# Optimization experiments

Measured on AMD Instinct MI355X. Metric: run time of the kernel, lower is better.

## Reference

```python
import jax, jax.numpy as jnp
import numpy as np

D_MODEL = 2048
NUM_HEADS = 16
D_K = D_MODEL // NUM_HEADS
THETA = 10000.0
BATCH, SEQ = 2, 2048


def setup_inputs() -> dict:
    key = jax.random.key(0)
    ks = jax.random.split(key, 5)
    scale = 1.0 / np.sqrt(D_MODEL)
    x = jax.random.normal(ks[0], (BATCH, SEQ, D_MODEL), dtype=jnp.float32)
    token_positions = jnp.broadcast_to(jnp.arange(SEQ, dtype=jnp.int32)[None, :], (BATCH, SEQ))
    Wq = jax.random.normal(ks[1], (D_MODEL, D_MODEL), dtype=jnp.float32) * scale
    Wk = jax.random.normal(ks[2], (D_MODEL, D_MODEL), dtype=jnp.float32) * scale
    Wv = jax.random.normal(ks[3], (D_MODEL, D_MODEL), dtype=jnp.float32) * scale
    Wo = jax.random.normal(ks[4], (D_MODEL, D_MODEL), dtype=jnp.float32) * scale
    return {"x": x, "token_positions": token_positions, "Wq": Wq, "Wk": Wk, "Wv": Wv, "Wo": Wo}


def _apply_rope(t, positions):
    # t: [b, h, s, d_k]; positions: [b, s]. Interleaved-pair rotation.
    half = D_K // 2
    inv_freq = THETA ** (-jnp.arange(0, half, dtype=jnp.float32) * 2.0 / D_K)  # [half]
    ang = positions.astype(jnp.float32)[:, :, None] * inv_freq[None, None, :]  # [b, s, half]
    cos = jnp.cos(ang)[:, None, :, :]  # [b, 1, s, half]
    sin = jnp.sin(ang)[:, None, :, :]
    t2 = t.reshape(*t.shape[:-1], half, 2)
    x1, x2 = t2[..., 0], t2[..., 1]
    r1 = x1 * cos - x2 * sin
    r2 = x1 * sin + x2 * cos
    return jnp.stack([r1, r2], axis=-1).reshape(t.shape)


def reference(x, token_positions, Wq, Wk, Wv, Wo):
    b, s, _ = x.shape
    # Linear layers compute x @ W^T (weight stored as [out, in], no bias)
    def proj(w):
        y = jnp.einsum('bsd,ed->bse', x, w)
        return y.reshape(b, s, NUM_HEADS, D_K).transpose(0, 2, 1, 3)  # b h s d
    Q, K, V = proj(Wq), proj(Wk), proj(Wv)
    Q = _apply_rope(Q, token_positions)
    K = _apply_rope(K, token_positions)
    scores = jnp.einsum('bhqd,bhkd->bhqk', Q, K) / jnp.sqrt(jnp.float32(D_K))
    causal = jnp.tril(jnp.ones((s, s), dtype=bool))
    scores = jnp.where(causal[None, None], scores, jnp.finfo(scores.dtype).min)
    attn = jax.nn.softmax(scores, axis=-1)
    out = jnp.einsum('bhqk,bhkd->bhqd', attn, V)  # b h s d
    out = out.transpose(0, 2, 1, 3).reshape(b, s, D_MODEL)
    return jnp.einsum('bse,de->bsd', out, Wo)
```

## Files before the change

### kernel.cpp

```cpp
#include <hip/hip_runtime.h>
#include <cstdint>
#include <cstddef>

#define D_MODEL 2048
#define NHEAD 16
#define DK 128
#define SEQ 2048
#define BATCH 2
#define NTOK (BATCH * SEQ)
#define NQB 32

typedef __bf16 bf16;
typedef __bf16 bf16x2 __attribute__((ext_vector_type(2)));
typedef __bf16 bf16x4 __attribute__((ext_vector_type(4)));
typedef __bf16 bf16x8 __attribute__((ext_vector_type(8)));
typedef float f32x4 __attribute__((ext_vector_type(4)));

__device__ __forceinline__ void g2lds16(const void* g, void* l) {
  __builtin_amdgcn_global_load_lds(
      (const __attribute__((address_space(1))) void*)g,
      (__attribute__((address_space(3))) void*)l, 16, 0, 0);
}

__device__ __forceinline__ void cstore(float* p, float v) { *p = v; }
__device__ __forceinline__ void cstore(bf16* p, float v) { *p = (bf16)v; }

#define BAR()                              \
  {                                        \
    asm volatile("" ::: "memory");         \
    __builtin_amdgcn_s_barrier();          \
    asm volatile("" ::: "memory");         \
  }

__global__ void k_conv5(const float* __restrict__ X, const float* __restrict__ W0,
                        const float* __restrict__ W1, const float* __restrict__ W2,
                        const float* __restrict__ W3, bf16* __restrict__ xo,
                        bf16* __restrict__ o0, bf16* __restrict__ o1,
                        bf16* __restrict__ o2, bf16* __restrict__ o3,
                        int nx4, int nw4) {
  const float* in;
  bf16* out;
  int n;
  switch (blockIdx.y) {
    case 0: in = X; out = xo; n = nx4; break;
    case 1: in = W0; out = o0; n = nw4; break;
    case 2: in = W1; out = o1; n = nw4; break;
    case 3: in = W2; out = o2; n = nw4; break;
    default: in = W3; out = o3; n = nw4;
  }
  int i = blockIdx.x * blockDim.x + threadIdx.x;
  if (i >= n) return;
  const float4 v = ((const float4*)in)[i];
  bf16x4 o = {(bf16)v.x, (bf16)v.y, (bf16)v.z, (bf16)v.w};
  ((bf16x4*)out)[i] = o;
}

__global__ __launch_bounds__(512, 1) void k_gemm8(
    const bf16* __restrict__ A, const bf16* __restrict__ B0p, const bf16* __restrict__ B1p,
    const bf16* __restrict__ B2p, bf16* __restrict__ C0, bf16* __restrict__ C1,
    bf16* __restrict__ C2, const int* __restrict__ pos, int M, int N, int K) {
  const bf16* Bp = B0p;
  bf16* Cp = C0;
  if (blockIdx.z == 1) { Bp = B1p; Cp = C1; }
  else if (blockIdx.z == 2) { Bp = B2p; Cp = C2; }
  const bool rope = (blockIdx.z < 2);

  __shared__ bf16 Ab[2][256 * 64];
  __shared__ bf16 Bb[2][256 * 64];

  const int t = threadIdx.x;
  const int wid = t >> 6, lane = t & 63;
  const int wr = wid >> 2, wc = wid & 3;
  const int lr = lane & 15, lg = lane >> 4;
  const int bm = blockIdx.y, bn = blockIdx.x;
  const size_t arow0 = (size_t)bm * 256;
  const size_t brow0 = (size_t)bn * 256;

  const int srow = wid * 8 + (lane >> 3);
  const int schunk = ((lane & 7) ^ ((lane >> 3) & 7)) * 8;

#define STG(X, row0, k0, lb, h)                                                \
  {                                                                            \
    g2lds16(&(X)[((row0) + (h)*128 + srow) * (size_t)K + (k0) + schunk],       \
            &(lb)[((h)*128 + wid * 8) * 64]);                                  \
    g2lds16(&(X)[((row0) + (h)*128 + 64 + srow) * (size_t)K + (k0) + schunk],  \
            &(lb)[((h)*128 + 64 + wid * 8) * 64]);                             \
  }
#define LDA8(lb, mh, m, kk) \
  (*(const bf16x8*)&(lb)[((mh)*128 + wr * 64 + (m)*16 + lr) * 64 + ((((kk)*4 + lg) ^ (lr & 7)) * 8)])
#define LDB8(lb, nh, n, kk) \
  (*(const bf16x8*)&(lb)[((nh)*128 + wc * 32 + (n)*16 + lr) * 64 + ((((kk)*4 + lg) ^ (lr & 7)) * 8)])

  const int T = K >> 6;

  STG(A, arow0, 0, Ab[0], 0);
  STG(A, arow0, 0, Ab[0], 1);
  STG(Bp, brow0, 0, Bb[0], 0);
  STG(Bp, brow0, 0, Bb[0], 1);
  STG(A, arow0, 64, Ab[1], 0);

  f32x4 acc[2][2][4][2] = {};

  for (int tt = 0; tt < T; ++tt) {
    const int cur = tt & 1;
    const bf16* Ac = Ab[cur];
    const bf16* Bc = Bb[cur];
    bf16* Aw = Ab[cur];
    bf16* An = Ab[cur ^ 1];
    bf16* Bn = Bb[cur ^ 1];
    const int k1 = (tt + 1) << 6;
    const int k2 = (tt + 2) << 6;
    const bool pf1 = (tt + 1 < T);
    const bool pf2 = (tt + 2 < T);

    if (tt == T - 1) {
      asm volatile("s_waitcnt vmcnt(0)" ::: "memory");
    } else {
      asm volatile("s_waitcnt vmcnt(2)" ::: "memory");
    }
    BAR();

    bf16x8 a[4][2], b0[2][2], b1[2][2];

#pragma unroll
    for (int m = 0; m < 4; ++m)
#pragma unroll
      for (int kk = 0; kk < 2; ++kk) a[m][kk] = LDA8(Ac, 0, m, kk);
#pragma unroll
    for (int n = 0; n < 2; ++n)
#pragma unroll
      for (int kk = 0; kk < 2; ++kk) b0[n][kk] = LDB8(Bc, 0, n, kk);
    if (pf1) {
      STG(A, arow0, k1, An, 1);
      STG(Bp, brow0, k1, Bn, 0);
    }
    __builtin_amdgcn_s_setprio(1);
#pragma unroll
    for (int m = 0; m < 4; ++m)
#pragma unroll
      for (int n = 0; n < 2; ++n)
#pragma unroll
        for (int kk = 0; kk < 2; ++kk)
          acc[0][0][m][n] =
              __builtin_amdgcn_mfma_f32_16x16x32_bf16(a[m][kk], b0[n][kk], acc[0][0][m][n], 0, 0, 0);
    __builtin_amdgcn_s_setprio(0);
    BAR();

#pragma unroll
    for (int n = 0; n < 2; ++n)
#pragma unroll
      for (int kk = 0; kk < 2; ++kk) b1[n][kk] = LDB8(Bc, 1, n, kk);
    if (pf1) STG(Bp, brow0, k1, Bn, 1);
    __builtin_amdgcn_s_setprio(1);
#pragma unroll
    for (int m = 0; m < 4; ++m)
#pragma unroll
      for (int n = 0; n < 2; ++n)
#pragma unroll
        for (int kk = 0; kk < 2; ++kk)
          acc[0][1][m][n] =
              __builtin_amdgcn_mfma_f32_16x16x32_bf16(a[m][kk], b1[n][kk], acc[0][1][m][n], 0, 0, 0);
    __builtin_amdgcn_s_setprio(0);

#pragma unroll
    for (int m = 0; m < 4; ++m)
#pragma unroll
      for (int kk = 0; kk < 2; ++kk) a[m][kk] = LDA8(Ac, 1, m, kk);
    if (pf2) STG(A, arow0, k2, Aw, 0);
    __builtin_amdgcn_s_setprio(1);
#pragma unroll
    for (int m = 0; m < 4; ++m)
#pragma unroll
      for (int n = 0; n < 2; ++n)
#pragma unroll
        for (int kk = 0; kk < 2; ++kk)
          acc[1][1][m][n] =
              __builtin_amdgcn_mfma_f32_16x16x32_bf16(a[m][kk], b1[n][kk], acc[1][1][m][n], 0, 0, 0);

#pragma unroll
    for (int m = 0; m < 4; ++m)
#pragma unroll
      for (int n = 0; n < 2; ++n)
#pragma unroll
        for (int kk = 0; kk < 2; ++kk)
          acc[1][0][m][n] =
              __builtin_amdgcn_mfma_f32_16x16x32_bf16(a[m][kk], b0[n][kk], acc[1][0][m][n], 0, 0, 0);
    __builtin_amdgcn_s_setprio(0);
  }

  float invf[2];
#pragma unroll
  for (int n = 0; n < 2; ++n) {
    int f = ((wc * 32 + n * 16 + lr) & 127) >> 1;
    invf[n] = exp2f((float)f * -0.20762050593121503f);
  }
#pragma unroll
  for (int mh = 0; mh < 2; ++mh)
#pragma unroll
    for (int m = 0; m < 4; ++m) {
      size_t rowb = arow0 + mh * 128 + wr * 64 + m * 16 + lg * 4;
#pragma unroll
      for (int r = 0; r < 4; ++r) {
        float p = rope ? (float)pos[rowb + r] : 0.0f;
#pragma unroll
        for (int n = 0; n < 2; ++n) {
          float sn, cs;
          if (rope) __sincosf(p * invf[n], &sn, &cs);
#pragma unroll
          for (int nh = 0; nh < 2; ++nh) {
            float v = acc[mh][nh][m][n][r];
            float vp = __shfl_xor(v, 1);
            float outv = v;
            if (rope) outv = (lr & 1) ? (v * cs + vp * sn) : (v * cs - vp * sn);
            size_t col = brow0 + nh * 128 + wc * 32 + n * 16 + lr;
            Cp[(rowb + r) * N + col] = (bf16)outv;
          }
        }
      }
    }
#undef STG
#undef LDA8
#undef LDB8
}

__global__ __launch_bounds__(512, 1) void k_gemmPV(
    const bf16* __restrict__ A, const bf16* __restrict__ Bp, bf16* __restrict__ Cp,
    int M, int N, int K) {
  const int wg = blockIdx.x;
  const int bn = wg & 7;
  const int bm = wg >> 3;

  __shared__ bf16 Ab[2][128 * 64];
  __shared__ bf16 Bb[2][256 * 64];

  const int t = threadIdx.x;
  const int wid = t >> 6, lane = t & 63;
  const int wr = wid >> 2, wc = wid & 3;
  const int lr = lane & 15, lg = lane >> 4;
  const size_t arow0 = (size_t)bm * 128;
  const size_t brow0 = (size_t)bn * 256;

  const int srow = wid * 8 + (lane >> 3);
  const int schunk = ((lane & 7) ^ ((lane >> 3) & 7)) * 8;

#define STGA(X, k0, lb, h) \
  g2lds16(&(X)[(arow0 + (h)*64 + srow) * (size_t)K + (k0) + schunk], &(lb)[((h)*64 + wid * 8) * 64]);
#define STGB(X, k0, lb, h)                                                        \
  {                                                                               \
    g2lds16(&(X)[(brow0 + (h)*128 + srow) * (size_t)K + (k0) + schunk],           \
            &(lb)[((h)*128 + wid * 8) * 64]);                                     \
    g2lds16(&(X)[(brow0 + (h)*128 + 64 + srow) * (size_t)K + (k0) + schunk],      \
            &(lb)[((h)*128 + 64 + wid * 8) * 64]);                                \
  }
#define LDA8(lb, mh, m, kk) \
  (*(const bf16x8*)&(lb)[((mh)*64 + wr * 32 + (m)*16 + lr) * 64 + ((((kk)*4 + lg) ^ (lr & 7)) * 8)])
#define LDB8(lb, nh, n, kk) \
  (*(const bf16x8*)&(lb)[((nh)*128 + wc * 32 + (n)*16 + lr) * 64 + ((((kk)*4 + lg) ^ (lr & 7)) * 8)])

  const int T = K >> 6;

  STGA(A, 0, Ab[0], 0);
  STGA(A, 0, Ab[0], 1);
  STGB(Bp, 0, Bb[0], 0);
  STGB(Bp, 0, Bb[0], 1);
  STGA(A, 64, Ab[1], 0);

  f32x4 acc[2][2][2][2] = {};

  for (int tt = 0; tt < T; ++tt) {
    const int cur = tt & 1;
    const bf16* Ac = Ab[cur];
    const bf16* Bc = Bb[cur];
    bf16* Aw = Ab[cur];
    bf16* An = Ab[cur ^ 1];
    bf16* Bn = Bb[cur ^ 1];
    const int k1 = (tt + 1) << 6;
    const int k2 = (tt + 2) << 6;
    const bool pf1 = (tt + 1 < T);
    const bool pf2 = (tt + 2 < T);

    if (tt == T - 1) {
      asm volatile("s_waitcnt vmcnt(0)" ::: "memory");
    } else {
      asm volatile("s_waitcnt vmcnt(1)" ::: "memory");
    }
    BAR();

    bf16x8 a[2][2], b[2][2];

#pragma unroll
    for (int m = 0; m < 2; ++m)
#pragma unroll
      for (int kk = 0; kk < 2; ++kk) a[m][kk] = LDA8(Ac, 0, m, kk);
#pragma unroll
    for (int n = 0; n < 2; ++n)
#pragma unroll
      for (int kk = 0; kk < 2; ++kk) b[n][kk] = LDB8(Bc, 0, n, kk);
    if (pf1) {
      STGA(A, k1, An, 1);
      STGB(Bp, k1, Bn, 0);
    }
    __builtin_amdgcn_s_setprio(1);
#pragma unroll
    for (int m = 0; m < 2; ++m)
#pragma unroll
      for (int n = 0; n < 2; ++n)
#pragma unroll
        for (int kk = 0; kk < 2; ++kk)
          acc[0][0][m][n] =
              __builtin_amdgcn_mfma_f32_16x16x32_bf16(a[m][kk], b[n][kk], acc[0][0][m][n], 0, 0, 0);
    __builtin_amdgcn_s_setprio(0);
    BAR();

#pragma unroll
    for (int n = 0; n < 2; ++n)
#pragma unroll
      for (int kk = 0; kk < 2; ++kk) b[n][kk] = LDB8(Bc, 1, n, kk);
    if (pf1) STGB(Bp, k1, Bn, 1);
    __builtin_amdgcn_s_setprio(1);
#pragma unroll
    for (int m = 0; m < 2; ++m)
#pragma unroll
      for (int n = 0; n < 2; ++n)
#pragma unroll
        for (int kk = 0; kk < 2; ++kk)
          acc[0][1][m][n] =
              __builtin_amdgcn_mfma_f32_16x16x32_bf16(a[m][kk], b[n][kk], acc[0][1][m][n], 0, 0, 0);
    __builtin_amdgcn_s_setprio(0);
    BAR();

#pragma unroll
    for (int m = 0; m < 2; ++m)
#pragma unroll
      for (int kk = 0; kk < 2; ++kk) a[m][kk] = LDA8(Ac, 1, m, kk);
    if (pf2) STGA(A, k2, Aw, 0);
    __builtin_amdgcn_s_setprio(1);
#pragma unroll
    for (int m = 0; m < 2; ++m)
#pragma unroll
      for (int n = 0; n < 2; ++n)
#pragma unroll
        for (int kk = 0; kk < 2; ++kk)
          acc[1][1][m][n] =
              __builtin_amdgcn_mfma_f32_16x16x32_bf16(a[m][kk], b[n][kk], acc[1][1][m][n], 0, 0, 0);
    __builtin_amdgcn_s_setprio(0);
    BAR();

#pragma unroll
    for (int n = 0; n < 2; ++n)
#pragma unroll
      for (int kk = 0; kk < 2; ++kk) b[n][kk] = LDB8(Bc, 0, n, kk);
    __builtin_amdgcn_s_setprio(1);
#pragma unroll
    for (int m = 0; m < 2; ++m)
#pragma unroll
      for (int n = 0; n < 2; ++n)
#pragma unroll
        for (int kk = 0; kk < 2; ++kk)
          acc[1][0][m][n] =
              __builtin_amdgcn_mfma_f32_16x16x32_bf16(a[m][kk], b[n][kk], acc[1][0][m][n], 0, 0, 0);
    __builtin_amdgcn_s_setprio(0);
  }

#pragma unroll
  for (int mh = 0; mh < 2; ++mh)
#pragma unroll
    for (int nh = 0; nh < 2; ++nh)
#pragma unroll
      for (int m = 0; m < 2; ++m) {
        size_t rowb = arow0 + mh * 64 + wr * 32 + m * 16 + lg * 4;
#pragma unroll
        for (int n = 0; n < 2; ++n) {
          size_t col = brow0 + nh * 128 + wc * 32 + n * 16 + lr;
#pragma unroll
          for (int r = 0; r < 4; ++r) Cp[(rowb + r) * N + col] = (bf16)acc[mh][nh][m][n][r];
        }
      }
#undef STGA
#undef STGB
#undef LDA8
#undef LDB8
}

template <typename OutT>
__global__ __launch_bounds__(256, 2) void k_gemm_nt(
    const bf16* __restrict__ A, const bf16* __restrict__ B0, const bf16* __restrict__ B1,
    const bf16* __restrict__ B2, OutT* __restrict__ C0, OutT* __restrict__ C1,
    OutT* __restrict__ C2, int M, int N, int K) {
  const bf16* Bp = B0;
  OutT* Cp = C0;
  if (blockIdx.z == 1) { Bp = B1; Cp = C1; }
  else if (blockIdx.z == 2) { Bp = B2; Cp = C2; }

  __shared__ bf16 As[128 * 32];
  __shared__ bf16 Bs[128 * 32];

  const int t = threadIdx.x;
  const int w = t >> 6;
  const int lane = t & 63;
  const int lr = lane & 15;
  const int lg = lane >> 4;
  const int wr = w >> 1, wc = w & 1;
  const int bm = blockIdx.y, bn = blockIdx.x;

  f32x4 acc[4][4] = {};

  const int srow = lane >> 2;
  const int scol = (lane & 3) * 8;

  const int kt_iters = K >> 5;
  for (int kt = 0; kt < kt_iters; ++kt) {
    const int kbase = kt * 32;
#pragma unroll
    for (int i = 0; i < 2; ++i) {
      int chunk = w * 2 + i;
      int row = chunk * 16 + srow;
      g2lds16(&A[(size_t)(bm * 128 + row) * K + kbase + scol], &As[chunk * 512]);
      g2lds16(&Bp[(size_t)(bn * 128 + row) * K + kbase + scol], &Bs[chunk * 512]);
    }
    asm volatile("s_waitcnt vmcnt(0)" ::: "memory");
    __syncthreads();

    bf16x8 af[4], bfr[4];
#pragma unroll
    for (int m = 0; m < 4; ++m)
      af[m] = *(const bf16x8*)&As[(wr * 64 + m * 16 + lr) * 32 + lg * 8];
#pragma unroll
    for (int n = 0; n < 4; ++n)
      bfr[n] = *(const bf16x8*)&Bs[(wc * 64 + n * 16 + lr) * 32 + lg * 8];
#pragma unroll
    for (int m = 0; m < 4; ++m)
#pragma unroll
      for (int n = 0; n < 4; ++n)
        acc[m][n] = __builtin_amdgcn_mfma_f32_16x16x32_bf16(af[m], bfr[n], acc[m][n], 0, 0, 0);
    __syncthreads();
  }

#pragma unroll
  for (int m = 0; m < 4; ++m) {
    int rowb = bm * 128 + wr * 64 + m * 16 + lg * 4;
#pragma unroll
    for (int n = 0; n < 4; ++n) {
      int col = bn * 128 + wc * 64 + n * 16 + lr;
#pragma unroll
      for (int r = 0; r < 4; ++r) cstore(&Cp[(size_t)(rowb + r) * N + col], acc[m][n][r]);
    }
  }
}

__global__ __launch_bounds__(256, 2) void k_attn(const bf16* __restrict__ Q,
                                                 const bf16* __restrict__ K,
                                                 const bf16* __restrict__ V,
                                                 bf16* __restrict__ O) {
  const int wg = blockIdx.x;
  const int g = wg & 7;
  const int i = wg >> 3;
  const int bh = g + 8 * (i & 3);
  const int pr = i >> 2;
  const int b = bh >> 4, h = bh & 15;

  const int t = threadIdx.x;
  const int w = t >> 6, lane = t & 63;
  const int lr = lane & 15, lg = lane >> 4;

  const size_t rowbase = (size_t)b * SEQ;
  const int hoff = h * DK;

  __shared__ bf16 Ks[2][64 * 128];
  __shared__ uint32_t VTu[2][128 * 32];
  __shared__ bf16 Pb[4][16 * 64];

  const int kp = t & 31;
  const int d0s = (t >> 5) * 16;

  const float scale = 0.08838834764831845f;
  const float FIXM = 8.0f;

  bf16x8 sa0, sa1, sb0, sb1;
  int cur = 0;

  const int krow_l = lane >> 4;
  const int kchunk = lane & 15;

  for (int qsel = 0; qsel < 2; ++qsel) {
    const int qblk = qsel ? pr : (NQB - 1 - pr);
    const int qb = qblk * 64;
    const int ktiles = qblk + 1;

    bf16x8 qf[4];
    {
      size_t qrow = rowbase + qb + w * 16 + lr;
#pragma unroll
      for (int c = 0; c < 4; ++c)
        qf[c] = *(const bf16x8*)&Q[qrow * D_MODEL + hoff + c * 32 + lg * 8];
    }

    f32x4 o[8] = {};
    f32x4 lrow = {};

#pragma unroll
    for (int j = 0; j < 4; ++j) {
      int row = w * 16 + j * 4 + krow_l;
      int chunk = kchunk ^ (j * 4 + krow_l);
      g2lds16(&K[(rowbase + row) * D_MODEL + hoff + chunk * 8],
              &Ks[cur][(size_t)(w * 16 + j * 4) * 128]);
    }
    {
      const bf16* vp0 = &V[(rowbase + 2 * kp) * D_MODEL + hoff + d0s];
      sa0 = *(const bf16x8*)vp0;
      sa1 = *(const bf16x8*)(vp0 + 8);
      sb0 = *(const bf16x8*)(vp0 + D_MODEL);
      sb1 = *(const bf16x8*)(vp0 + D_MODEL + 8);
    }

    for (int kt = 0; kt < ktiles; ++kt) {
      const int k0 = kt * 64;
#pragma unroll
      for (int j = 0; j < 8; ++j) {
        int d = d0s + j;
        bf16x2 p0 = {sa0[j], sb0[j]};
        VTu[cur][d * 32 + (kp ^ ((d & 7) << 2))] = *(const uint32_t*)&p0;
      }
#pragma unroll
      for (int j = 0; j < 8; ++j) {
        int d = d0s + 8 + j;
        bf16x2 p1 = {sa1[j], sb1[j]};
        VTu[cur][d * 32 + (kp ^ ((d & 7) << 2))] = *(const uint32_t*)&p1;
      }
      asm volatile("s_waitcnt vmcnt(0)" ::: "memory");
      __syncthreads();

      if (kt + 1 < ktiles) {
#pragma unroll
        for (int j = 0; j < 4; ++j) {
          int row = w * 16 + j * 4 + krow_l;
          int chunk = kchunk ^ (j * 4 + krow_l);
          g2lds16(&K[(rowbase + k0 + 64 + row) * D_MODEL + hoff + chunk * 8],
                  &Ks[cur ^ 1][(size_t)(w * 16 + j * 4) * 128]);
        }
        const bf16* vp0 = &V[(rowbase + k0 + 64 + 2 * kp) * D_MODEL + hoff + d0s];
        sa0 = *(const bf16x8*)vp0;
        sa1 = *(const bf16x8*)(vp0 + 8);
        sb0 = *(const bf16x8*)(vp0 + D_MODEL);
        sb1 = *(const bf16x8*)(vp0 + D_MODEL + 8);
      }

      f32x4 sc[4];
      __builtin_amdgcn_s_setprio(1);
#pragma unroll
      for (int tt = 0; tt < 4; ++tt) {
        f32x4 a = {};
#pragma unroll
        for (int c = 0; c < 4; ++c) {
          bf16x8 kf = *(const bf16x8*)&Ks[cur][(tt * 16 + lr) * 128 + (((c * 4 + lg) ^ lr) * 8)];
          a = __builtin_amdgcn_mfma_f32_16x16x32_bf16(qf[c], kf, a, 0, 0, 0);
        }
        sc[tt] = a * scale;
      }
      __builtin_amdgcn_s_setprio(0);

      const int qrow0 = qb + w * 16 + lg * 4;
      if (k0 + 64 > qb + w * 16) {
#pragma unroll
        for (int tt = 0; tt < 4; ++tt) {
          int kcol = k0 + tt * 16 + lr;
#pragma unroll
          for (int r = 0; r < 4; ++r)
            if (kcol > qrow0 + r) sc[tt][r] = -3.0e38f;
        }
      }

#pragma unroll
      for (int tt = 0; tt < 4; ++tt)
#pragma unroll
        for (int r = 0; r < 4; ++r) {
          float p = __expf(sc[tt][r] - FIXM);
          sc[tt][r] = p;
          lrow[r] += p;
        }

#pragma unroll
      for (int tt = 0; tt < 4; ++tt)
#pragma unroll
        for (int r = 0; r < 4; ++r) {
          int q = lg * 4 + r;
          int col = tt * 16 + lr;
          Pb[w][q * 64 + (col ^ ((q & 7) << 3))] = (bf16)sc[tt][r];
        }
      asm volatile("s_waitcnt lgkmcnt(0)" ::: "memory");
      bf16x8 pf0 = *(const bf16x8*)&Pb[w][lr * 64 + ((lg * 8) ^ ((lr & 7) << 3))];
      bf16x8 pf1 = *(const bf16x8*)&Pb[w][lr * 64 + ((32 + lg * 8) ^ ((lr & 7) << 3))];

      __builtin_amdgcn_s_setprio(1);
#pragma unroll
      for (int nt = 0; nt < 8; ++nt) {
        int d = nt * 16 + lr;
        bf16x8 vf0 = *(const bf16x8*)&VTu[cur][d * 32 + ((lg * 4) ^ ((d & 7) << 2))];
        bf16x8 vf1 = *(const bf16x8*)&VTu[cur][d * 32 + ((16 + lg * 4) ^ ((d & 7) << 2))];
        o[nt] = __builtin_amdgcn_mfma_f32_16x16x32_bf16(pf0, vf0, o[nt], 0, 0, 0);
        o[nt] = __builtin_amdgcn_mfma_f32_16x16x32_bf16(pf1, vf1, o[nt], 0, 0, 0);
      }
      __builtin_amdgcn_s_setprio(0);
      cur ^= 1;
    }

#pragma unroll
    for (int off = 8; off >= 1; off >>= 1)
#pragma unroll
      for (int r = 0; r < 4; ++r) lrow[r] += __shfl_xor(lrow[r], off);

    size_t orow = rowbase + qb + w * 16 + lg * 4;
#pragma unroll
    for (int nt = 0; nt < 8; ++nt)
#pragma unroll
      for (int r = 0; r < 4; ++r)
        O[(orow + r) * D_MODEL + hoff + nt * 16 + lr] = (bf16)(o[nt][r] / lrow[r]);
  }
}

extern "C" void kernel_launch(void* const* d_in, const int* in_sizes, int n_in, void* d_out,
                              int out_size, void* d_ws, size_t ws_size, hipStream_t stream) {
  const float* x = (const float*)d_in[0];
  const int* pos = (const int*)d_in[1];
  const float* Wq = (const float*)d_in[2];
  const float* Wk = (const float*)d_in[3];
  const float* Wv = (const float*)d_in[4];
  const float* Wo = (const float*)d_in[5];
  float* out = (float*)d_out;

  char* ws = (char*)d_ws;
  const size_t MB = 1u << 20;
  bf16* xb  = (bf16*)(ws);
  bf16* wqb = (bf16*)(ws + 16 * MB);
  bf16* wkb = (bf16*)(ws + 24 * MB);
  bf16* wvb = (bf16*)(ws + 32 * MB);
  bf16* wob = (bf16*)(ws + 40 * MB);
  bf16* Qb  = (bf16*)(ws + 48 * MB);
  bf16* Kb  = (bf16*)(ws + 64 * MB);
  bf16* Vb  = (bf16*)(ws + 80 * MB);
  bf16* AOb = (bf16*)(ws + 96 * MB);

  {
    int nx4 = NTOK * D_MODEL / 4;
    int nw4 = D_MODEL * D_MODEL / 4;
    k_conv5<<<dim3((nx4 + 255) / 256, 5), 256, 0, stream>>>(
        x, Wq, Wk, Wv, Wo, xb, wqb, wkb, wvb, wob, nx4, nw4);
  }
  {
    dim3 g(D_MODEL / 256, NTOK / 256, 2);
    k_gemm8<<<g, 512, 0, stream>>>(xb, wqb, wkb, wkb, Qb, Kb, Kb, pos,
                                   NTOK, D_MODEL, D_MODEL);
  }
  k_gemmPV<<<256, 512, 0, stream>>>(xb, wvb, Vb, NTOK, D_MODEL, D_MODEL);
  k_attn<<<dim3(NQB * NHEAD * BATCH / 2, 1, 1), 256, 0, stream>>>(Qb, Kb, Vb, AOb);
  {
    dim3 g(D_MODEL / 128, NTOK / 128, 1);
    k_gemm_nt<float><<<g, 256, 0, stream>>>(AOb, wob, wob, wob, out, out, out, NTOK, D_MODEL, D_MODEL);
  }
}
```

Baseline: 261.7 us.

## Pre-transpose V into a per-head global buffer and stage it with async LDS loads

Adds a k_vtrans kernel that writes V transposed per batch-head into a [bh][d][seq] buffer, reusing the x workspace, which is safe because x is consumed by then. The attention kernel then loads V tiles straight into LDS with async global_load_lds and an XOR swizzle. This replaces the in-register pack and transposed LDS stores of V that ran inside the attention loop. The cost is an extra kernel launch plus an extra read and write of V (16 MB of bf16 traffic).

```diff
diff --git a/kernel.cpp b/kernel.cpp
--- a/kernel.cpp
+++ b/kernel.cpp
@@ -382,6 +382,31 @@
 #undef LDB8
 }
 
+__global__ __launch_bounds__(256, 4) void k_vtrans(const bf16* __restrict__ V,
+                                                   bf16* __restrict__ VT) {
+  const int bh = blockIdx.z;
+  const int b = bh >> 4, h = bh & 15;
+  const int tt64 = blockIdx.x * 64;
+  const int t = threadIdx.x;
+  __shared__ bf16 L[128][72];
+  const int tok_l = t & 63, dc0 = t >> 6;
+#pragma unroll
+  for (int p = 0; p < 4; ++p) {
+    int dc = dc0 * 4 + p;
+    bf16x8 v = *(const bf16x8*)&V[((size_t)(b * SEQ) + tt64 + tok_l) * D_MODEL + h * DK + dc * 8];
+#pragma unroll
+    for (int j = 0; j < 8; ++j) L[dc * 8 + j][tok_l] = v[j];
+  }
+  __syncthreads();
+  const int d = t >> 1, half = t & 1;
+  const size_t obase = ((size_t)bh * DK + d) * SEQ + tt64;
+#pragma unroll
+  for (int i = 0; i < 4; ++i) {
+    int g = half * 4 + i;
+    *(bf16x8*)&VT[obase + g * 8] = *(const bf16x8*)&L[d][g * 8];
+  }
+}
+
 template <typename OutT>
 __global__ __launch_bounds__(256, 2) void k_gemm_nt(
     const bf16* __restrict__ A, const bf16* __restrict__ B0, const bf16* __restrict__ B1,
@@ -450,7 +475,7 @@
 
 __global__ __launch_bounds__(256, 2) void k_attn(const bf16* __restrict__ Q,
                                                  const bf16* __restrict__ K,
-                                                 const bf16* __restrict__ V,
+                                                 const bf16* __restrict__ VT,
                                                  bf16* __restrict__ O) {
   const int wg = blockIdx.x;
   const int g = wg & 7;
@@ -465,22 +490,36 @@
 
   const size_t rowbase = (size_t)b * SEQ;
   const int hoff = h * DK;
+  const size_t vtbase = (size_t)bh * DK * SEQ;
 
   __shared__ bf16 Ks[2][64 * 128];
-  __shared__ uint32_t VTu[2][128 * 32];
+  __shared__ bf16 VTb[2][128 * 64];
   __shared__ bf16 Pb[4][16 * 64];
-
-  const int kp = t & 31;
-  const int d0s = (t >> 5) * 16;
 
   const float scale = 0.08838834764831845f;
   const float FIXM = 8.0f;
 
-  bf16x8 sa0, sa1, sb0, sb1;
   int cur = 0;
 
   const int krow_l = lane >> 4;
   const int kchunk = lane & 15;
+  const int vrow_l = lane >> 3;
+  const int vchunk = lane & 7;
+
+#define STGK(k0v, buf)                                                         \
+  _Pragma("unroll") for (int j_ = 0; j_ < 4; ++j_) {                           \
+    int row_ = w * 16 + j_ * 4 + krow_l;                                       \
+    int ck_ = kchunk ^ (row_ & 15);                                            \
+    g2lds16(&K[(rowbase + (k0v) + row_) * D_MODEL + hoff + ck_ * 8],           \
+            &Ks[buf][(size_t)(w * 16 + j_ * 4) * 128]);                        \
+  }
+#define STGV(k0v, buf)                                                         \
+  _Pragma("unroll") for (int j_ = 0; j_ < 4; ++j_) {                           \
+    int d_ = w * 32 + j_ * 8 + vrow_l;                                         \
+    int ck_ = vchunk ^ (d_ & 7);                                               \
+    g2lds16(&VT[vtbase + (size_t)d_ * SEQ + (k0v) + ck_ * 8],                  \
+            &VTb[buf][(size_t)(w * 32 + j_ * 8) * 64]);                        \
+  }
 
   for (int qsel = 0; qsel < 2; ++qsel) {
     const int qblk = qsel ? pr : (NQB - 1 - pr);
@@ -498,51 +537,17 @@
     f32x4 o[8] = {};
     f32x4 lrow = {};
 
-#pragma unroll
-    for (int j = 0; j < 4; ++j) {
-      int row = w * 16 + j * 4 + krow_l;
-      int chunk = kchunk ^ (j * 4 + krow_l);
-      g2lds16(&K[(rowbase + row) * D_MODEL + hoff + chunk * 8],
-              &Ks[cur][(size_t)(w * 16 + j * 4) * 128]);
-    }
-    {
-      const bf16* vp0 = &V[(rowbase + 2 * kp) * D_MODEL + hoff + d0s];
-      sa0 = *(const bf16x8*)vp0;
-      sa1 = *(const bf16x8*)(vp0 + 8);
-      sb0 = *(const bf16x8*)(vp0 + D_MODEL);
-      sb1 = *(const bf16x8*)(vp0 + D_MODEL + 8);
-    }
+    STGK(0, cur);
+    STGV(0, cur);
 
     for (int kt = 0; kt < ktiles; ++kt) {
       const int k0 = kt * 64;
-#pragma unroll
-      for (int j = 0; j < 8; ++j) {
-        int d = d0s + j;
-        bf16x2 p0 = {sa0[j], sb0[j]};
-        VTu[cur][d * 32 + (kp ^ ((d & 7) << 2))] = *(const uint32_t*)&p0;
-      }
-#pragma unroll
-      for (int j = 0; j < 8; ++j) {
-        int d = d0s + 8 + j;
-        bf16x2 p1 = {sa1[j], sb1[j]};
-        VTu[cur][d * 32 + (kp ^ ((d & 7) << 2))] = *(const uint32_t*)&p1;
-      }
       asm volatile("s_waitcnt vmcnt(0)" ::: "memory");
       __syncthreads();
 
       if (kt + 1 < ktiles) {
-#pragma unroll
-        for (int j = 0; j < 4; ++j) {
-          int row = w * 16 + j * 4 + krow_l;
-          int chunk = kchunk ^ (j * 4 + krow_l);
-          g2lds16(&K[(rowbase + k0 + 64 + row) * D_MODEL + hoff + chunk * 8],
-                  &Ks[cur ^ 1][(size_t)(w * 16 + j * 4) * 128]);
-        }
-        const bf16* vp0 = &V[(rowbase + k0 + 64 + 2 * kp) * D_MODEL + hoff + d0s];
-        sa0 = *(const bf16x8*)vp0;
-        sa1 = *(const bf16x8*)(vp0 + 8);
-        sb0 = *(const bf16x8*)(vp0 + D_MODEL);
-        sb1 = *(const bf16x8*)(vp0 + D_MODEL + 8);
+        STGK(k0 + 64, cur ^ 1);
+        STGV(k0 + 64, cur ^ 1);
       }
 
       f32x4 sc[4];
@@ -595,8 +600,8 @@
 #pragma unroll
       for (int nt = 0; nt < 8; ++nt) {
         int d = nt * 16 + lr;
-        bf16x8 vf0 = *(const bf16x8*)&VTu[cur][d * 32 + ((lg * 4) ^ ((d & 7) << 2))];
-        bf16x8 vf1 = *(const bf16x8*)&VTu[cur][d * 32 + ((16 + lg * 4) ^ ((d & 7) << 2))];
+        bf16x8 vf0 = *(const bf16x8*)&VTb[cur][d * 64 + ((lg ^ (d & 7)) * 8)];
+        bf16x8 vf1 = *(const bf16x8*)&VTb[cur][d * 64 + (((4 + lg) ^ (d & 7)) * 8)];
         o[nt] = __builtin_amdgcn_mfma_f32_16x16x32_bf16(pf0, vf0, o[nt], 0, 0, 0);
         o[nt] = __builtin_amdgcn_mfma_f32_16x16x32_bf16(pf1, vf1, o[nt], 0, 0, 0);
       }
@@ -616,6 +621,8 @@
       for (int r = 0; r < 4; ++r)
         O[(orow + r) * D_MODEL + hoff + nt * 16 + lr] = (bf16)(o[nt][r] / lrow[r]);
   }
+#undef STGK
+#undef STGV
 }
 
 extern "C" void kernel_launch(void* const* d_in, const int* in_sizes, int n_in, void* d_out,
@@ -639,6 +646,7 @@
   bf16* Kb  = (bf16*)(ws + 64 * MB);
   bf16* Vb  = (bf16*)(ws + 80 * MB);
   bf16* AOb = (bf16*)(ws + 96 * MB);
+  bf16* VTg = xb;
 
   {
     int nx4 = NTOK * D_MODEL / 4;
@@ -652,7 +660,8 @@
                                    NTOK, D_MODEL, D_MODEL);
   }
   k_gemmPV<<<256, 512, 0, stream>>>(xb, wvb, Vb, NTOK, D_MODEL, D_MODEL);
-  k_attn<<<dim3(NQB * NHEAD * BATCH / 2, 1, 1), 256, 0, stream>>>(Qb, Kb, Vb, AOb);
+  k_vtrans<<<dim3(SEQ / 64, 1, BATCH * NHEAD), 256, 0, stream>>>(Vb, VTg);
+  k_attn<<<dim3(NQB * NHEAD * BATCH / 2, 1, 1), 256, 0, stream>>>(Qb, Kb, VTg, AOb);
   {
     dim3 g(D_MODEL / 128, NTOK / 128, 1);
     k_gemm_nt<float><<<g, 256, 0, stream>>>(AOb, wob, wob, wob, out, out, out, NTOK, D_MODEL, D_MODEL);
```

After: 262.7 us. No clear change (+0.4%).
